# Kernel tuning notes

Measured on AMD Instinct MI355X. Metric: run time of the kernel, lower is better.

The kernel has to match this reference:

```python
import jax, jax.numpy as jnp
import numpy as np

L, B, T, F, C, H, DFF = 2, 4, 2048, 1024, 200, 8, 128


def setup_inputs() -> dict:
    key = jax.random.key(0)
    ks = jax.random.split(key, 12)
    s = 0.02
    return {
        "x": jax.random.normal(ks[0], (B, T, F), jnp.float32),
        "prototypes": jax.random.normal(ks[1], (C, 1, F), jnp.float32),
        # conv_query / conv_key (1x1 convs == linear), per RAB layer
        "wq": jax.random.normal(ks[2], (L, F, F), jnp.float32) * s,
        "bq": jnp.zeros((L, F), jnp.float32),
        "wk": jax.random.normal(ks[3], (L, F, F), jnp.float32) * s,
        "bk": jnp.zeros((L, F), jnp.float32),
        # nn.MultiheadAttention packed in-proj and out-proj
        "in_w": jax.random.normal(ks[4], (L, 3 * F, F), jnp.float32) * s,
        "in_b": jnp.zeros((L, 3 * F), jnp.float32),
        "out_w": jax.random.normal(ks[5], (L, F, F), jnp.float32) * s,
        "out_b": jnp.zeros((L, F), jnp.float32),
        # FFN
        "l1_w": jax.random.normal(ks[6], (L, DFF, F), jnp.float32) * s,
        "l1_b": jnp.zeros((L, DFF), jnp.float32),
        "l2_w": jax.random.normal(ks[7], (L, F, DFF), jnp.float32) * s,
        "l2_b": jnp.zeros((L, F), jnp.float32),
        # LayerNorms
        "ln1_g": jnp.ones((L, F), jnp.float32),
        "ln1_b": jnp.zeros((L, F), jnp.float32),
        "ln2_g": jnp.ones((L, F), jnp.float32),
        "ln2_b": jnp.zeros((L, F), jnp.float32),
        # feature_embedding: Conv1d(F, F, k=3, pad=1) + ReLU
        "emb_w": jax.random.normal(ks[8], (F, F, 3), jnp.float32) * s,
        "emb_b": jnp.zeros((F,), jnp.float32),
    }


def _ln(x, g, b, eps=1e-5):
    mu = jnp.mean(x, axis=-1, keepdims=True)
    var = jnp.mean((x - mu) ** 2, axis=-1, keepdims=True)
    return (x - mu) * jax.lax.rsqrt(var + eps) * g + b


def _mha(q, k, v, w, b, ow, ob):
    # q,k,v: (B,S,F). Packed in-proj like nn.MultiheadAttention (eval: no dropout).
    f = q.shape[-1]
    dh = f // H
    Q = q @ w[:f].T + b[:f]
    K = k @ w[f:2 * f].T + b[f:2 * f]
    V = v @ w[2 * f:].T + b[2 * f:]
    sp = lambda t: t.reshape(t.shape[0], t.shape[1], H, dh)
    scale = np.float32(1.0 / np.sqrt(dh))
    att = jnp.einsum('bqhd,bkhd->bhqk', sp(Q), sp(K)) * scale
    att = jax.nn.softmax(att, axis=-1)
    o = jnp.einsum('bhqk,bkhd->bqhd', att, sp(V)).reshape(q.shape)
    return o @ ow.T + ob


def reference(x, prototypes, wq, bq, wk, bk, in_w, in_b, out_w, out_b,
              l1_w, l1_b, l2_w, l2_b, ln1_g, ln1_b, ln2_g, ln2_b, emb_w, emb_b):
    Bn, Tn, Fn = x.shape
    # torch: prototypes.view(1, F, -1)  (a reshape, NOT a transpose)
    proto = jnp.broadcast_to(prototypes.reshape(1, Fn, -1), (Bn, Fn, prototypes.shape[0]))
    # concat along time: (B,F,S) with S = T + C, then work in (B,S,F)
    src = jnp.swapaxes(jnp.concatenate([jnp.swapaxes(x, 1, 2), proto], axis=2), 1, 2)
    for l in range(L):
        q = src @ wq[l].T + bq[l]          # conv1x1 == pointwise linear
        k = src @ wk[l].T + bk[l]
        a = _mha(q, k, src, in_w[l], in_b[l], out_w[l], out_b[l])
        src = _ln(src + a, ln1_g[l], ln1_b[l])
        ff = jax.nn.relu(src @ l1_w[l].T + l1_b[l]) @ l2_w[l].T + l2_b[l]
        src = _ln(src + ff, ln2_g[l], ln2_b[l])
    feat = jnp.swapaxes(src[:, :Tn], 1, 2)  # (B,F,T): drop prototype tokens
    y = jax.lax.conv_general_dilated(feat, emb_w, (1,), ((1, 1),),
                                     dimension_numbers=('NCH', 'OIH', 'NCH'))
    return jax.nn.relu(y + emb_b[None, :, None])
```

## Files before the change

### kernel.cpp

```cpp
#include <hip/hip_runtime.h>
#include <hip/hip_bf16.h>


constexpr int BN = 4, TN = 2048, FD = 1024, CP = 200, SN = TN + CP;
constexpr int HN = 8, DH = 128, DF = 128, MR = BN * SN;
constexpr int SF = 3 * FD;
constexpr int NT = (SN + 63) / 64;
constexpr float C2 = 0.12751744f;

typedef __attribute__((ext_vector_type(8))) short short8;
typedef __attribute__((ext_vector_type(4))) float f32x4;

__device__ __forceinline__ ushort f2b(float f) {
  union { float f; uint u; } v{f};
  return (ushort)((v.u + 0x7fffu + ((v.u >> 16) & 1u)) >> 16);
}
__device__ __forceinline__ float b2f(ushort u) {
  union { uint u; float f; } v{(uint)u << 16};
  return v.f;
}
__device__ __forceinline__ uint cvt_pk_bf16(float a, float b) {
  uint r;
  asm("v_cvt_pk_bf16_f32 %0, %1, %2" : "=v"(r) : "v"(a), "v"(b));
  return r;
}
__device__ __forceinline__ float exp2_fast(float x) {
  float r;
  asm("v_exp_f32 %0, %1" : "=v"(r) : "v"(x));
  return r;
}
__device__ __forceinline__ void gld16(const void* g, void* l) {
  __builtin_amdgcn_global_load_lds(
      (const __attribute__((address_space(1))) void*)g,
      (__attribute__((address_space(3))) void*)l, 16, 0, 0);
}

__global__ __launch_bounds__(256) void k_build(const float* __restrict__ x,
                                               const float* __restrict__ proto,
                                               ushort* __restrict__ srcb) {
  const int row = blockIdx.x;
  const int b = row / SN, s = row % SN;
  const int f = threadIdx.x * 4;
  const size_t o = (size_t)row * FD + f;
  float4 v;
  if (s < TN) {
    v = *(const float4*)(x + ((size_t)b * TN + s) * FD + f);
  } else {
    const int c = s - TN;
    v.x = proto[(size_t)(f + 0) * CP + c];
    v.y = proto[(size_t)(f + 1) * CP + c];
    v.z = proto[(size_t)(f + 2) * CP + c];
    v.w = proto[(size_t)(f + 3) * CP + c];
  }
  ushort4 u{f2b(v.x), f2b(v.y), f2b(v.z), f2b(v.w)};
  *(ushort4*)(srcb + o) = u;
}

__global__ __launch_bounds__(256) void k_cvt(const float* __restrict__ in,
                                             ushort* __restrict__ out, int n) {
  const int n4 = n >> 2;
  for (int i = blockIdx.x * 256 + threadIdx.x; i < n4; i += gridDim.x * 256) {
    const float4 v = *(const float4*)(in + (size_t)i * 4);
    ushort4 u{f2b(v.x), f2b(v.y), f2b(v.z), f2b(v.w)};
    *(ushort4*)(out + (size_t)i * 4) = u;
  }
}

__global__ __launch_bounds__(256) void k_cvt_inw(const float* __restrict__ in,
                                                 ushort* __restrict__ wInQK,
                                                 ushort* __restrict__ wQKV) {
  constexpr size_t FF = (size_t)FD * FD;
  const int n4 = (int)(6 * FF / 4);
  for (int i = blockIdx.x * 256 + threadIdx.x; i < n4; i += gridDim.x * 256) {
    const size_t idx = (size_t)i * 4;
    const float4 v = *(const float4*)(in + idx);
    ushort4 u{f2b(v.x), f2b(v.y), f2b(v.z), f2b(v.w)};
    const int l = (int)(idx / (3 * FF));
    const size_t r = idx % (3 * FF);
    ushort* dst = (r >= 2 * FF) ? (wQKV + l * 3 * FF + r)
                                : (wInQK + l * 2 * FF + r);
    *(ushort4*)dst = u;
  }
}

__global__ __launch_bounds__(256) void k_cvtT(const float* __restrict__ wq,
                                              const float* __restrict__ wk,
                                              ushort* __restrict__ wT) {
  const int z = blockIdx.z;
  const int qk = z >> 1, l = z & 1;
  const float* W = (qk ? wk : wq) + (size_t)l * FD * FD;
  ushort* WT = wT + (size_t)z * FD * FD;
  __shared__ float t[32][33];
  const int tx = threadIdx.x & 31, ty = threadIdx.x >> 5;
  const int x0 = blockIdx.x * 32, y0 = blockIdx.y * 32;
#pragma unroll
  for (int dy = 0; dy < 4; ++dy)
    t[ty + dy * 8][tx] = W[(size_t)(y0 + ty + dy * 8) * FD + x0 + tx];
  __syncthreads();
#pragma unroll
  for (int dy = 0; dy < 4; ++dy)
    WT[(size_t)(x0 + ty + dy * 8) * FD + y0 + tx] = f2b(t[tx][ty + dy * 8]);
}

__global__ __launch_bounds__(256) void k_vT(const ushort* __restrict__ V,
                                            ushort* __restrict__ Vt) {
  __shared__ ushort t[32][34];
  const int tx = threadIdx.x & 31, ty = threadIdx.x >> 5;
  const int s0 = blockIdx.x * 32, d0 = blockIdx.y * 32, bh = blockIdx.z;
  const int b = bh >> 3, h = bh & 7;
#pragma unroll
  for (int dy = 0; dy < 4; ++dy) {
    const int s = min(s0 + ty + dy * 8, SN - 1);
    t[ty + dy * 8][tx] = V[((size_t)b * SN + s) * SF + h * DH + d0 + tx];
  }
  __syncthreads();
#pragma unroll
  for (int dy = 0; dy < 4; ++dy) {
    const int s = s0 + tx;
    if (s < SN)
      Vt[((size_t)bh * DH + d0 + ty + dy * 8) * SN + s] = t[tx][ty + dy * 8];
  }
}

__global__ __launch_bounds__(256) void k_convw(const float* __restrict__ W,
                                               ushort* __restrict__ out) {
  const int n = FD * FD * 3;
  for (int idx = blockIdx.x * 256 + threadIdx.x; idx < n;
       idx += gridDim.x * 256) {
    const int o = idx / (FD * 3);
    const int rem = idx % (FD * 3);
    const int tau = rem >> 10, i = rem & 1023;
    out[idx] = f2b(W[(size_t)o * (FD * 3) + i * 3 + tau]);
  }
}

__global__ __launch_bounds__(256) void k_pad(const ushort* __restrict__ sb,
                                             ushort* __restrict__ pad) {
  const int r = blockIdx.x, b = blockIdx.y;
  const int f = threadIdx.x * 4;
  ushort4 v{0, 0, 0, 0};
  if (r >= 1 && r <= TN)
    v = *(const ushort4*)(sb + ((size_t)b * SN + (r - 1)) * FD + f);
  *(ushort4*)(pad + ((size_t)b * (TN + 2) + r) * FD + f) = v;
}

__global__ __launch_bounds__(256) void k_beff(const float* __restrict__ in_w,
                                              const float* __restrict__ bvec,
                                              const float* __restrict__ in_b,
                                              float* __restrict__ out, int qk) {
  const int n = blockIdx.x, l = blockIdx.y, tid = threadIdx.x;
  const float* Win = in_w + (size_t)(l * 3 + qk) * FD * FD;
  const float* bv = bvec + (size_t)l * FD;
  float s = 0.f;
  for (int j = tid; j < FD; j += 256) s += Win[(size_t)n * FD + j] * bv[j];
  __shared__ float red[4];
#pragma unroll
  for (int o = 32; o; o >>= 1) s += __shfl_xor(s, o);
  if ((tid & 63) == 0) red[tid >> 6] = s;
  __syncthreads();
  if (tid == 0)
    out[l * 3 * FD + qk * FD + n] =
        red[0] + red[1] + red[2] + red[3] + in_b[l * 3 * FD + qk * FD + n];
}

__global__ __launch_bounds__(256) void k_copyv(const float* __restrict__ in_b,
                                               float* __restrict__ bqkv) {
  const int l = blockIdx.y;
  const int i = blockIdx.x * 256 + threadIdx.x;
  bqkv[l * 3 * FD + 2 * FD + i] = in_b[l * 3 * FD + 2 * FD + i];
}

template <bool RELU, bool BF16OUT, bool PREP4 = false>
__global__ __launch_bounds__(256) void k_mm(const ushort* __restrict__ A,
                                            const ushort* __restrict__ W,
                                            const float* __restrict__ bias,
                                            void* __restrict__ Cv,
                                            int M, int N, int K) {
  constexpr size_t FF = (size_t)FD * FD;
  if (PREP4) {
    const int z = blockIdx.z;
    A += (size_t)z * FF;
    W += (size_t)(((z & 1) * 2) + (z >> 1)) * FF;
    Cv = (void*)((ushort*)Cv + (size_t)((z >> 1) * 3 + (z & 1)) * FF);
  }
  __shared__ __align__(16) ushort As[128 * 32];
  __shared__ __align__(16) ushort Ws[128 * 32];
  const int tid = threadIdx.x;
  const int lane = tid & 63, wv = tid >> 6;
  const int l15 = lane & 15, g = lane >> 4;
  const int wr = wv >> 1, wc = wv & 1;
  int bx = blockIdx.x, by = blockIdx.y;
  const int nwg = gridDim.x * gridDim.y;
  if ((nwg & 7) == 0) {
    int bid = by * gridDim.x + bx;
    bid = (bid & 7) * (nwg >> 3) + (bid >> 3);
    bx = bid % gridDim.x;
    by = bid / gridDim.x;
  }
  const int m0 = by * 128, n0 = bx * 128;
  f32x4 acc[4][4];
#pragma unroll
  for (int i = 0; i < 4; ++i)
#pragma unroll
    for (int j = 0; j < 4; ++j) acc[i][j] = (f32x4){0.f, 0.f, 0.f, 0.f};

  for (int k0 = 0; k0 < K; k0 += 32) {
#pragma unroll
    for (int j = 0; j < 2; ++j) {
      const int u = j * 256 + wv * 64 + lane;
      const int r = u >> 2, c = (u & 3) * 8;
      const int gm = min(m0 + r, M - 1);
      gld16(A + (size_t)gm * K + k0 + c, As + (size_t)u * 8);
    }
#pragma unroll
    for (int j = 0; j < 2; ++j) {
      const int u = j * 256 + wv * 64 + lane;
      const int r = u >> 2, c = (u & 3) * 8;
      gld16(W + (size_t)(n0 + r) * K + k0 + c, Ws + (size_t)u * 8);
    }
    __syncthreads();
    short8 af[4], bfr[4];
#pragma unroll
    for (int i = 0; i < 4; ++i)
      af[i] = *(const short8*)(As + (wr * 64 + i * 16 + l15) * 32 + g * 8);
#pragma unroll
    for (int j = 0; j < 4; ++j)
      bfr[j] = *(const short8*)(Ws + (wc * 64 + j * 16 + l15) * 32 + g * 8);
    __builtin_amdgcn_s_setprio(1);
#pragma unroll
    for (int i = 0; i < 4; ++i)
#pragma unroll
      for (int j = 0; j < 4; ++j)
        acc[i][j] = __builtin_amdgcn_mfma_f32_16x16x32_bf16(af[i], bfr[j],
                                                            acc[i][j], 0, 0, 0);
    __builtin_amdgcn_s_setprio(0);
    __syncthreads();
  }
#pragma unroll
  for (int i = 0; i < 4; ++i) {
#pragma unroll
    for (int r = 0; r < 4; ++r) {
      const int row = m0 + wr * 64 + i * 16 + g * 4 + r;
      if (row >= M) continue;
#pragma unroll
      for (int j = 0; j < 4; ++j) {
        const int col = n0 + wc * 64 + j * 16 + l15;
        float v = acc[i][j][r];
        if (bias) v += bias[col];
        if (RELU) v = fmaxf(v, 0.f);
        if (BF16OUT)
          ((ushort*)Cv)[(size_t)row * N + col] = f2b(v);
        else
          ((float*)Cv)[(size_t)row * N + col] = v;
      }
    }
  }
}

template <bool CONV, bool BF16OUT>
__global__ __launch_bounds__(512, 1) void k_mmB(const ushort* __restrict__ A,
                                                const ushort* __restrict__ W,
                                                const float* __restrict__ bias,
                                                void* __restrict__ Cv,
                                                int M, int N, int K) {
  __shared__ __align__(16) ushort As[2][128 * 64];
  __shared__ __align__(16) ushort Bs[2][256 * 64];
  const int tid = threadIdx.x;
  const int lane = tid & 63, wv = tid >> 6;
  const int l15 = lane & 15, g = lane >> 4;
  const int wr = wv >> 2, wc = wv & 3;
  int bx = blockIdx.x, by = blockIdx.y;
  const int nwg = gridDim.x * gridDim.y;
  if ((nwg & 7) == 0) {
    int bid = by * gridDim.x + bx;
    bid = (bid & 7) * (nwg >> 3) + (bid >> 3);
    bx = bid % gridDim.x;
    by = bid / gridDim.x;
  }
  const int m0 = by * 128, n0 = bx * 256;
  const int NKt = K >> 6;

  f32x4 acc[4][4];
#pragma unroll
  for (int i = 0; i < 4; ++i)
#pragma unroll
    for (int j = 0; j < 4; ++j) acc[i][j] = (f32x4){0.f, 0.f, 0.f, 0.f};

  auto stage = [&](int kt, int d) {
    const int kb = kt * 64;
#pragma unroll
    for (int j = 0; j < 2; ++j) {
      const int u = j * 512 + tid;
      const int row = u >> 3, s = u & 7;
      const int c = s ^ (row & 7);
      const ushort* ga;
      if (CONV) {
        const int rm = m0 + row;
        const int bb = rm >> 11, tt = rm & 2047;
        ga = A + (size_t)(bb * (TN + 2) + tt + (kb >> 10)) * FD + (kb & 1023) +
             c * 8;
      } else {
        ga = A + (size_t)min(m0 + row, M - 1) * K + kb + c * 8;
      }
      gld16(ga, As[d] + row * 64 + s * 8);
    }
#pragma unroll
    for (int j = 0; j < 4; ++j) {
      const int u = j * 512 + tid;
      const int row = u >> 3, s = u & 7;
      const int c = s ^ (row & 7);
      gld16(W + (size_t)(n0 + row) * K + kb + c * 8, Bs[d] + row * 64 + s * 8);
    }
  };

  stage(0, 0);
  for (int kt = 0; kt < NKt; ++kt) {
    const int cur = kt & 1;
    if (kt + 1 < NKt) {
      stage(kt + 1, cur ^ 1);
      asm volatile("s_waitcnt vmcnt(6)" ::: "memory");
    } else {
      asm volatile("s_waitcnt vmcnt(0)" ::: "memory");
    }
    __builtin_amdgcn_s_barrier();
    __builtin_amdgcn_sched_barrier(0);
#pragma unroll
    for (int ks = 0; ks < 2; ++ks) {
      short8 aq[4], bq[4];
#pragma unroll
      for (int mf = 0; mf < 4; ++mf) {
        const int row = wr * 64 + mf * 16 + l15;
        aq[mf] = *(const short8*)(As[cur] + row * 64 +
                                  (((ks * 4 + g) ^ (row & 7)) << 3));
      }
#pragma unroll
      for (int nf = 0; nf < 4; ++nf) {
        const int row = wc * 64 + nf * 16 + l15;
        bq[nf] = *(const short8*)(Bs[cur] + row * 64 +
                                  (((ks * 4 + g) ^ (row & 7)) << 3));
      }
      __builtin_amdgcn_s_setprio(1);
#pragma unroll
      for (int mf = 0; mf < 4; ++mf)
#pragma unroll
        for (int nf = 0; nf < 4; ++nf)
          acc[mf][nf] = __builtin_amdgcn_mfma_f32_16x16x32_bf16(
              aq[mf], bq[nf], acc[mf][nf], 0, 0, 0);
      __builtin_amdgcn_s_setprio(0);
    }
    asm volatile("s_waitcnt lgkmcnt(0)" ::: "memory");
    __builtin_amdgcn_s_barrier();
  }

#pragma unroll
  for (int mf = 0; mf < 4; ++mf) {
#pragma unroll
    for (int r = 0; r < 4; ++r) {
      const int row = m0 + wr * 64 + mf * 16 + g * 4 + r;
      if (!CONV && row >= M) continue;
#pragma unroll
      for (int nf = 0; nf < 4; ++nf) {
        const int col = n0 + wc * 64 + nf * 16 + l15;
        float v = acc[mf][nf][r];
        if (bias) v += bias[col];
        if (CONV) {
          v = fmaxf(v, 0.f);
          const int bb = row >> 11, tt = row & 2047;
          ((float*)Cv)[((size_t)(bb * FD + col)) * TN + tt] = v;
        } else if (BF16OUT) {
          ((ushort*)Cv)[(size_t)row * N + col] = f2b(v);
        } else {
          ((float*)Cv)[(size_t)row * N + col] = v;
        }
      }
    }
  }
}

__global__ __launch_bounds__(512) void k_fattn(const ushort* __restrict__ Qg,
                                               const ushort* __restrict__ Kg,
                                               const ushort* __restrict__ Vt,
                                               ushort* __restrict__ Og) {
  __shared__ __align__(16) ushort Ks[64 * 128];
  __shared__ __align__(16) ushort Vs[128 * 64];
  __shared__ __align__(16) ushort Ps[8][16 * 64];
  const int tid = threadIdx.x, lane = tid & 63, wv = tid >> 6;
  const int l15 = lane & 15, g = lane >> 4;
  const int b = blockIdx.z, h = blockIdx.y, q0 = blockIdx.x * 128;
  const size_t rowBase = (size_t)b * SN;
  const int hoff = h * DH;
  const size_t vbase = (size_t)(b * HN + h) * DH * SN;

  short8 qf[4];
  const int qrow = min(q0 + wv * 16 + l15, SN - 1);
#pragma unroll
  for (int c = 0; c < 4; ++c)
    qf[c] = *(const short8*)(Qg + (rowBase + qrow) * SF + hoff + c * 32 + g * 8);

  short8 onesf;
#pragma unroll
  for (int i = 0; i < 8; ++i) onesf[i] = (short)0x3F80;

  f32x4 o[8];
#pragma unroll
  for (int dt = 0; dt < 8; ++dt) o[dt] = (f32x4){0.f, 0.f, 0.f, 0.f};
  f32x4 lacc = (f32x4){0.f, 0.f, 0.f, 0.f};
  const char* KsB = (const char*)Ks;
  const char* VsB = (const char*)Vs;
  char* PsB = (char*)&Ps[wv][0];

  for (int t = 0; t < NT; ++t) {
    const int kv0 = t * 64;
    const bool tl = (t == NT - 1);
    if (tl) {
#pragma unroll
      for (int j = 0; j < 2; ++j) {
        const int su = j * 512 + tid;
        const int row = su >> 4, s = su & 15;
        const int c16 = s ^ (row & 7);
        const int krow = min(kv0 + row, SN - 1);
        gld16(Kg + (rowBase + krow) * SF + hoff + c16 * 8, Ks + (size_t)su * 8);
      }
#pragma unroll
      for (int j = 0; j < 2; ++j) {
        const int su = j * 512 + tid;
        const int row = su >> 3, s = su & 7;
        const int cc = s ^ (row & 7);
        const int kvc = min(kv0 + cc * 8, SN - 8);
        gld16(Vt + vbase + (size_t)row * SN + kvc, Vs + (size_t)su * 8);
      }
    } else {
#pragma unroll
      for (int j = 0; j < 2; ++j) {
        const int su = j * 512 + tid;
        const int row = su >> 4, s = su & 15;
        const int c16 = s ^ (row & 7);
        gld16(Kg + (rowBase + kv0 + row) * SF + hoff + c16 * 8,
              Ks + (size_t)su * 8);
      }
#pragma unroll
      for (int j = 0; j < 2; ++j) {
        const int su = j * 512 + tid;
        const int row = su >> 3, s = su & 7;
        const int cc = s ^ (row & 7);
        gld16(Vt + vbase + (size_t)row * SN + kv0 + cc * 8,
              Vs + (size_t)su * 8);
      }
    }
    __syncthreads();

    f32x4 st[4];
    __builtin_amdgcn_s_setprio(1);
#pragma unroll
    for (int kt = 0; kt < 4; ++kt) {
      f32x4 s4 = (f32x4){0.f, 0.f, 0.f, 0.f};
      const int row = kt * 16 + l15;
#pragma unroll
      for (int c = 0; c < 4; ++c) {
        const short8 kf = *(const short8*)(
            KsB + row * 256 + (((c * 4 + g) ^ (row & 7)) << 4));
        s4 = __builtin_amdgcn_mfma_f32_16x16x32_bf16(kf, qf[c], s4, 0, 0, 0);
      }
      st[kt] = s4;
    }
    __builtin_amdgcn_s_setprio(0);

    float pfl[16];
    if (tl) {
#pragma unroll
      for (int kt = 0; kt < 4; ++kt)
#pragma unroll
        for (int r = 0; r < 4; ++r) {
          const int kvg = kv0 + kt * 16 + g * 4 + r;
          pfl[kt * 4 + r] = (kvg < SN) ? exp2_fast(C2 * st[kt][r]) : 0.f;
        }
    } else {
#pragma unroll
      for (int i = 0; i < 16; ++i)
        pfl[i] = exp2_fast(C2 * st[i >> 2][i & 3]);
    }

#pragma unroll
    for (int kt = 0; kt < 4; ++kt) {
      const uint lo = cvt_pk_bf16(pfl[kt * 4 + 0], pfl[kt * 4 + 1]);
      const uint hi = cvt_pk_bf16(pfl[kt * 4 + 2], pfl[kt * 4 + 3]);
      const int slot = (kt * 2 + (g >> 1)) ^ (l15 & 7);
      *(uint2*)(PsB + l15 * 128 + slot * 16 + (g & 1) * 8) = make_uint2(lo, hi);
    }

    __builtin_amdgcn_s_setprio(1);
#pragma unroll
    for (int c2 = 0; c2 < 2; ++c2) {
      const int pslot = (c2 * 4 + g) ^ (l15 & 7);
      const short8 pf = *(const short8*)(PsB + l15 * 128 + pslot * 16);
      lacc = __builtin_amdgcn_mfma_f32_16x16x32_bf16(pf, onesf, lacc, 0, 0, 0);
#pragma unroll
      for (int dt = 0; dt < 8; ++dt) {
        const int row = dt * 16 + l15;
        const short8 vf = *(const short8*)(
            VsB + row * 128 + (((c2 * 4 + g) ^ (row & 7)) << 4));
        o[dt] = __builtin_amdgcn_mfma_f32_16x16x32_bf16(pf, vf, o[dt], 0, 0, 0);
      }
    }
    __builtin_amdgcn_s_setprio(0);
    __syncthreads();
  }

  float ir[4];
#pragma unroll
  for (int r = 0; r < 4; ++r) ir[r] = 1.f / lacc[r];
#pragma unroll
  for (int r = 0; r < 4; ++r) {
    const int orow = q0 + wv * 16 + g * 4 + r;
    if (orow >= SN) continue;
#pragma unroll
    for (int dt = 0; dt < 8; ++dt)
      Og[(rowBase + orow) * FD + hoff + dt * 16 + l15] = f2b(o[dt][r] * ir[r]);
  }
}

__global__ __launch_bounds__(256) void k_add_ln(ushort* __restrict__ sb,
                                                const ushort* __restrict__ d,
                                                const float* __restrict__ g,
                                                const float* __restrict__ be) {
  __shared__ float red[4];
  const int row = blockIdx.x;
  const int tid = threadIdx.x;
  const int c = tid * 4;
  const size_t off = (size_t)row * FD + c;
  const ushort4 sv = *(const ushort4*)(sb + off);
  const ushort4 dv = *(const ushort4*)(d + off);
  float v[4] = {b2f(sv.x) + b2f(dv.x), b2f(sv.y) + b2f(dv.y),
                b2f(sv.z) + b2f(dv.z), b2f(sv.w) + b2f(dv.w)};
  float sum = v[0] + v[1] + v[2] + v[3];
#pragma unroll
  for (int o = 32; o; o >>= 1) sum += __shfl_xor(sum, o);
  if ((tid & 63) == 0) red[tid >> 6] = sum;
  __syncthreads();
  sum = red[0] + red[1] + red[2] + red[3];
  const float mu = sum * (1.f / FD);
  float vs = 0.f;
#pragma unroll
  for (int i = 0; i < 4; ++i) {
    const float t = v[i] - mu;
    vs += t * t;
  }
  __syncthreads();
#pragma unroll
  for (int o = 32; o; o >>= 1) vs += __shfl_xor(vs, o);
  if ((tid & 63) == 0) red[tid >> 6] = vs;
  __syncthreads();
  vs = red[0] + red[1] + red[2] + red[3];
  const float rstd = rsqrtf(vs * (1.f / FD) + 1e-5f);
  const float4 gv = *(const float4*)(g + c);
  const float4 bv = *(const float4*)(be + c);
  ushort4 u{f2b((v[0] - mu) * rstd * gv.x + bv.x),
            f2b((v[1] - mu) * rstd * gv.y + bv.y),
            f2b((v[2] - mu) * rstd * gv.z + bv.z),
            f2b((v[3] - mu) * rstd * gv.w + bv.w)};
  *(ushort4*)(sb + off) = u;
}

extern "C" void kernel_launch(void* const* d_in, const int* in_sizes, int n_in,
                              void* d_out, int out_size, void* d_ws,
                              size_t ws_size, hipStream_t stream) {
  const float* x      = (const float*)d_in[0];
  const float* proto  = (const float*)d_in[1];
  const float* wq     = (const float*)d_in[2];
  const float* bq     = (const float*)d_in[3];
  const float* wk     = (const float*)d_in[4];
  const float* bk     = (const float*)d_in[5];
  const float* in_w   = (const float*)d_in[6];
  const float* in_b   = (const float*)d_in[7];
  const float* out_w  = (const float*)d_in[8];
  const float* out_b  = (const float*)d_in[9];
  const float* l1_w   = (const float*)d_in[10];
  const float* l1_b   = (const float*)d_in[11];
  const float* l2_w   = (const float*)d_in[12];
  const float* l2_b   = (const float*)d_in[13];
  const float* ln1_g  = (const float*)d_in[14];
  const float* ln1_b  = (const float*)d_in[15];
  const float* ln2_g  = (const float*)d_in[16];
  const float* ln2_b  = (const float*)d_in[17];
  const float* emb_w  = (const float*)d_in[18];
  const float* emb_b  = (const float*)d_in[19];

  char* p = (char*)d_ws;
  auto take = [&](size_t bytes) {
    char* r = p;
    p += (bytes + 255) & ~(size_t)255;
    return r;
  };
  const size_t MF = (size_t)MR * FD;
  const size_t FF = (size_t)FD * FD;
  ushort* srcb  = (ushort*)take(MF * 2);
  ushort* bQKV  = (ushort*)take((size_t)MR * SF * 2);
  ushort* bVt   = (ushort*)take((size_t)BN * HN * DH * SN * 2);
  ushort* bO    = (ushort*)take(MF * 2);
  ushort* bFF   = (ushort*)take((size_t)MR * DF * 2);
  ushort* wQKV  = (ushort*)take((size_t)2 * 3 * FF * 2);
  ushort* wOut  = (ushort*)take((size_t)2 * FF * 2);
  ushort* wL1   = (ushort*)take((size_t)2 * DF * FD * 2);
  ushort* wL2   = (ushort*)take((size_t)2 * FD * DF * 2);
  float*  bqkv  = (float*)take((size_t)2 * SF * 4);
  ushort* wT     = bQKV;
  ushort* wInQK  = bQKV + 4 * FF;
  ushort* bOut   = bQKV;
  ushort* srcPad = bQKV;
  ushort* convW  = bQKV + (size_t)10 * 1024 * 1024;

  k_build<<<MR, 256, 0, stream>>>(x, proto, srcb);
  k_cvt_inw<<<2048, 256, 0, stream>>>(in_w, wInQK, wQKV);
  k_cvt<<<1024, 256, 0, stream>>>(out_w, wOut, 2 * FF);
  k_cvt<<<256, 256, 0, stream>>>(l1_w, wL1, 2 * DF * FD);
  k_cvt<<<256, 256, 0, stream>>>(l2_w, wL2, 2 * FD * DF);
  k_cvtT<<<dim3(32, 32, 4), 256, 0, stream>>>(wq, wk, wT);
  k_mm<false, true, true><<<dim3(8, 8, 4), 256, 0, stream>>>(
      wInQK, wT, nullptr, wQKV, FD, FD, FD);
  k_beff<<<dim3(FD, 2), 256, 0, stream>>>(in_w, bq, in_b, bqkv, 0);
  k_beff<<<dim3(FD, 2), 256, 0, stream>>>(in_w, bk, in_b, bqkv, 1);
  k_copyv<<<dim3(4, 2), 256, 0, stream>>>(in_b, bqkv);

  const int MB = (MR + 127) / 128;

  for (int l = 0; l < 2; ++l) {
    k_mmB<false, true><<<dim3(SF / 256, MB), 512, 0, stream>>>(
        srcb, wQKV + (size_t)l * 3 * FF, bqkv + (size_t)l * SF, bQKV, MR, SF,
        FD);
    k_vT<<<dim3((SN + 31) / 32, DH / 32, BN * HN), 256, 0, stream>>>(
        bQKV + 2 * FD, bVt);
    k_fattn<<<dim3((SN + 127) / 128, HN, BN), 512, 0, stream>>>(
        bQKV, bQKV + FD, bVt, bO);
    k_mmB<false, true><<<dim3(FD / 256, MB), 512, 0, stream>>>(
        bO, wOut + (size_t)l * FF, out_b + (size_t)l * FD, bOut, MR, FD, FD);
    k_add_ln<<<MR, 256, 0, stream>>>(srcb, bOut, ln1_g + (size_t)l * FD,
                                     ln1_b + (size_t)l * FD);
    k_mm<true, true><<<dim3(DF / 128, MB), 256, 0, stream>>>(
        srcb, wL1 + (size_t)l * DF * FD, l1_b + (size_t)l * DF, bFF, MR, DF,
        FD);
    k_mm<false, true><<<dim3(FD / 128, MB), 256, 0, stream>>>(
        bFF, wL2 + (size_t)l * FD * DF, l2_b + (size_t)l * FD, bOut, MR, FD,
        DF);
    k_add_ln<<<MR, 256, 0, stream>>>(srcb, bOut, ln2_g + (size_t)l * FD,
                                     ln2_b + (size_t)l * FD);
  }

  k_convw<<<1024, 256, 0, stream>>>(emb_w, convW);
  k_pad<<<dim3(TN + 2, BN), 256, 0, stream>>>(srcb, srcPad);
  k_mmB<true, false><<<dim3(FD / 256, (BN * TN) / 128), 512, 0, stream>>>(
      srcPad, convW, emb_b, (float*)d_out, BN * TN, FD, 3 * FD);
}
```

Before: 0.9997 ms.

## Replace double-buffered 128x256 GEMM with simple 128x128 kernel and retile attention

Removes the 512-thread double-buffered k_mmB GEMM and routes the QKV, out-projection and conv GEMMs through the simpler single-buffered 256-thread 128x128 k_mm, which gains a CONV addressing mode. Flash attention moves from 128-query/512-thread blocks to 64-query/256-thread blocks, with an XCD-aware block remap so each (batch, head) group lands on one XCD. The bias kernels are merged into one launch. The changes trade software pipelining and larger tiles for more blocks and better cache locality, at the risk of exposing more global-load latency in the large GEMMs.

```diff
diff --git a/kernel.cpp b/kernel.cpp
--- a/kernel.cpp
+++ b/kernel.cpp
@@ -145,12 +145,19 @@
 }
 
 __global__ __launch_bounds__(256) void k_beff(const float* __restrict__ in_w,
-                                              const float* __restrict__ bvec,
+                                              const float* __restrict__ bq,
+                                              const float* __restrict__ bk,
                                               const float* __restrict__ in_b,
-                                              float* __restrict__ out, int qk) {
-  const int n = blockIdx.x, l = blockIdx.y, tid = threadIdx.x;
+                                              float* __restrict__ out) {
+  const int n = blockIdx.x, l = blockIdx.y, qk = blockIdx.z;
+  const int tid = threadIdx.x;
+  if (qk == 2) {
+    if (tid == 0)
+      out[l * 3 * FD + 2 * FD + n] = in_b[l * 3 * FD + 2 * FD + n];
+    return;
+  }
   const float* Win = in_w + (size_t)(l * 3 + qk) * FD * FD;
-  const float* bv = bvec + (size_t)l * FD;
+  const float* bv = (qk ? bk : bq) + (size_t)l * FD;
   float s = 0.f;
   for (int j = tid; j < FD; j += 256) s += Win[(size_t)n * FD + j] * bv[j];
   __shared__ float red[4];
@@ -163,14 +170,7 @@
         red[0] + red[1] + red[2] + red[3] + in_b[l * 3 * FD + qk * FD + n];
 }
 
-__global__ __launch_bounds__(256) void k_copyv(const float* __restrict__ in_b,
-                                               float* __restrict__ bqkv) {
-  const int l = blockIdx.y;
-  const int i = blockIdx.x * 256 + threadIdx.x;
-  bqkv[l * 3 * FD + 2 * FD + i] = in_b[l * 3 * FD + 2 * FD + i];
-}
-
-template <bool RELU, bool BF16OUT, bool PREP4 = false>
+template <bool RELU, bool BF16OUT, bool PREP4 = false, bool CONV = false>
 __global__ __launch_bounds__(256) void k_mm(const ushort* __restrict__ A,
                                             const ushort* __restrict__ W,
                                             const float* __restrict__ bias,
@@ -209,8 +209,16 @@
     for (int j = 0; j < 2; ++j) {
       const int u = j * 256 + wv * 64 + lane;
       const int r = u >> 2, c = (u & 3) * 8;
-      const int gm = min(m0 + r, M - 1);
-      gld16(A + (size_t)gm * K + k0 + c, As + (size_t)u * 8);
+      const ushort* ga;
+      if (CONV) {
+        const int rm = m0 + r;
+        const int bb = rm >> 11, tt = rm & 2047;
+        ga = A + (size_t)(bb * (TN + 2) + tt + (k0 >> 10)) * FD + (k0 & 1023) +
+             c;
+      } else {
+        ga = A + (size_t)min(m0 + r, M - 1) * K + k0 + c;
+      }
+      gld16(ga, As + (size_t)u * 8);
     }
 #pragma unroll
     for (int j = 0; j < 2; ++j) {
@@ -241,130 +249,14 @@
 #pragma unroll
     for (int r = 0; r < 4; ++r) {
       const int row = m0 + wr * 64 + i * 16 + g * 4 + r;
-      if (row >= M) continue;
+      if (!CONV && row >= M) continue;
 #pragma unroll
       for (int j = 0; j < 4; ++j) {
         const int col = n0 + wc * 64 + j * 16 + l15;
         float v = acc[i][j][r];
         if (bias) v += bias[col];
-        if (RELU) v = fmaxf(v, 0.f);
-        if (BF16OUT)
-          ((ushort*)Cv)[(size_t)row * N + col] = f2b(v);
-        else
-          ((float*)Cv)[(size_t)row * N + col] = v;
-      }
-    }
-  }
-}
-
-template <bool CONV, bool BF16OUT>
-__global__ __launch_bounds__(512, 1) void k_mmB(const ushort* __restrict__ A,
-                                                const ushort* __restrict__ W,
-                                                const float* __restrict__ bias,
-                                                void* __restrict__ Cv,
-                                                int M, int N, int K) {
-  __shared__ __align__(16) ushort As[2][128 * 64];
-  __shared__ __align__(16) ushort Bs[2][256 * 64];
-  const int tid = threadIdx.x;
-  const int lane = tid & 63, wv = tid >> 6;
-  const int l15 = lane & 15, g = lane >> 4;
-  const int wr = wv >> 2, wc = wv & 3;
-  int bx = blockIdx.x, by = blockIdx.y;
-  const int nwg = gridDim.x * gridDim.y;
-  if ((nwg & 7) == 0) {
-    int bid = by * gridDim.x + bx;
-    bid = (bid & 7) * (nwg >> 3) + (bid >> 3);
-    bx = bid % gridDim.x;
-    by = bid / gridDim.x;
-  }
-  const int m0 = by * 128, n0 = bx * 256;
-  const int NKt = K >> 6;
-
-  f32x4 acc[4][4];
-#pragma unroll
-  for (int i = 0; i < 4; ++i)
-#pragma unroll
-    for (int j = 0; j < 4; ++j) acc[i][j] = (f32x4){0.f, 0.f, 0.f, 0.f};
-
-  auto stage = [&](int kt, int d) {
-    const int kb = kt * 64;
-#pragma unroll
-    for (int j = 0; j < 2; ++j) {
-      const int u = j * 512 + tid;
-      const int row = u >> 3, s = u & 7;
-      const int c = s ^ (row & 7);
-      const ushort* ga;
-      if (CONV) {
-        const int rm = m0 + row;
-        const int bb = rm >> 11, tt = rm & 2047;
-        ga = A + (size_t)(bb * (TN + 2) + tt + (kb >> 10)) * FD + (kb & 1023) +
-             c * 8;
-      } else {
-        ga = A + (size_t)min(m0 + row, M - 1) * K + kb + c * 8;
-      }
-      gld16(ga, As[d] + row * 64 + s * 8);
-    }
-#pragma unroll
-    for (int j = 0; j < 4; ++j) {
-      const int u = j * 512 + tid;
-      const int row = u >> 3, s = u & 7;
-      const int c = s ^ (row & 7);
-      gld16(W + (size_t)(n0 + row) * K + kb + c * 8, Bs[d] + row * 64 + s * 8);
-    }
-  };
-
-  stage(0, 0);
-  for (int kt = 0; kt < NKt; ++kt) {
-    const int cur = kt & 1;
-    if (kt + 1 < NKt) {
-      stage(kt + 1, cur ^ 1);
-      asm volatile("s_waitcnt vmcnt(6)" ::: "memory");
-    } else {
-      asm volatile("s_waitcnt vmcnt(0)" ::: "memory");
-    }
-    __builtin_amdgcn_s_barrier();
-    __builtin_amdgcn_sched_barrier(0);
-#pragma unroll
-    for (int ks = 0; ks < 2; ++ks) {
-      short8 aq[4], bq[4];
-#pragma unroll
-      for (int mf = 0; mf < 4; ++mf) {
-        const int row = wr * 64 + mf * 16 + l15;
-        aq[mf] = *(const short8*)(As[cur] + row * 64 +
-                                  (((ks * 4 + g) ^ (row & 7)) << 3));
-      }
-#pragma unroll
-      for (int nf = 0; nf < 4; ++nf) {
-        const int row = wc * 64 + nf * 16 + l15;
-        bq[nf] = *(const short8*)(Bs[cur] + row * 64 +
-                                  (((ks * 4 + g) ^ (row & 7)) << 3));
-      }
-      __builtin_amdgcn_s_setprio(1);
-#pragma unroll
-      for (int mf = 0; mf < 4; ++mf)
-#pragma unroll
-        for (int nf = 0; nf < 4; ++nf)
-          acc[mf][nf] = __builtin_amdgcn_mfma_f32_16x16x32_bf16(
-              aq[mf], bq[nf], acc[mf][nf], 0, 0, 0);
-      __builtin_amdgcn_s_setprio(0);
-    }
-    asm volatile("s_waitcnt lgkmcnt(0)" ::: "memory");
-    __builtin_amdgcn_s_barrier();
-  }
-
-#pragma unroll
-  for (int mf = 0; mf < 4; ++mf) {
-#pragma unroll
-    for (int r = 0; r < 4; ++r) {
-      const int row = m0 + wr * 64 + mf * 16 + g * 4 + r;
-      if (!CONV && row >= M) continue;
-#pragma unroll
-      for (int nf = 0; nf < 4; ++nf) {
-        const int col = n0 + wc * 64 + nf * 16 + l15;
-        float v = acc[mf][nf][r];
-        if (bias) v += bias[col];
+        if (RELU || CONV) v = fmaxf(v, 0.f);
         if (CONV) {
-          v = fmaxf(v, 0.f);
           const int bb = row >> 11, tt = row & 2047;
           ((float*)Cv)[((size_t)(bb * FD + col)) * TN + tt] = v;
         } else if (BF16OUT) {
@@ -377,19 +269,23 @@
   }
 }
 
-__global__ __launch_bounds__(512) void k_fattn(const ushort* __restrict__ Qg,
+__global__ __launch_bounds__(256) void k_fattn(const ushort* __restrict__ Qg,
                                                const ushort* __restrict__ Kg,
                                                const ushort* __restrict__ Vt,
                                                ushort* __restrict__ Og) {
   __shared__ __align__(16) ushort Ks[64 * 128];
   __shared__ __align__(16) ushort Vs[128 * 64];
-  __shared__ __align__(16) ushort Ps[8][16 * 64];
+  __shared__ __align__(16) ushort Ps[4][16 * 64];
   const int tid = threadIdx.x, lane = tid & 63, wv = tid >> 6;
   const int l15 = lane & 15, g = lane >> 4;
-  const int b = blockIdx.z, h = blockIdx.y, q0 = blockIdx.x * 128;
+  const int flat = blockIdx.x + NT * (blockIdx.y + HN * blockIdx.z);
+  const int xcd = flat & 7, slot = flat >> 3;
+  const int grp = xcd + 8 * (slot / NT);
+  const int qt = slot % NT;
+  const int b = grp >> 3, h = grp & 7, q0 = qt * 64;
   const size_t rowBase = (size_t)b * SN;
   const int hoff = h * DH;
-  const size_t vbase = (size_t)(b * HN + h) * DH * SN;
+  const size_t vbase = (size_t)grp * DH * SN;
 
   short8 qf[4];
   const int qrow = min(q0 + wv * 16 + l15, SN - 1);
@@ -414,16 +310,16 @@
     const bool tl = (t == NT - 1);
     if (tl) {
 #pragma unroll
-      for (int j = 0; j < 2; ++j) {
-        const int su = j * 512 + tid;
+      for (int j = 0; j < 4; ++j) {
+        const int su = j * 256 + tid;
         const int row = su >> 4, s = su & 15;
         const int c16 = s ^ (row & 7);
         const int krow = min(kv0 + row, SN - 1);
         gld16(Kg + (rowBase + krow) * SF + hoff + c16 * 8, Ks + (size_t)su * 8);
       }
 #pragma unroll
-      for (int j = 0; j < 2; ++j) {
-        const int su = j * 512 + tid;
+      for (int j = 0; j < 4; ++j) {
+        const int su = j * 256 + tid;
         const int row = su >> 3, s = su & 7;
         const int cc = s ^ (row & 7);
         const int kvc = min(kv0 + cc * 8, SN - 8);
@@ -431,16 +327,16 @@
       }
     } else {
 #pragma unroll
-      for (int j = 0; j < 2; ++j) {
-        const int su = j * 512 + tid;
+      for (int j = 0; j < 4; ++j) {
+        const int su = j * 256 + tid;
         const int row = su >> 4, s = su & 15;
         const int c16 = s ^ (row & 7);
         gld16(Kg + (rowBase + kv0 + row) * SF + hoff + c16 * 8,
               Ks + (size_t)su * 8);
       }
 #pragma unroll
-      for (int j = 0; j < 2; ++j) {
-        const int su = j * 512 + tid;
+      for (int j = 0; j < 4; ++j) {
+        const int su = j * 256 + tid;
         const int row = su >> 3, s = su & 7;
         const int cc = s ^ (row & 7);
         gld16(Vt + vbase + (size_t)row * SN + kv0 + cc * 8,
@@ -617,21 +513,18 @@
   k_cvtT<<<dim3(32, 32, 4), 256, 0, stream>>>(wq, wk, wT);
   k_mm<false, true, true><<<dim3(8, 8, 4), 256, 0, stream>>>(
       wInQK, wT, nullptr, wQKV, FD, FD, FD);
-  k_beff<<<dim3(FD, 2), 256, 0, stream>>>(in_w, bq, in_b, bqkv, 0);
-  k_beff<<<dim3(FD, 2), 256, 0, stream>>>(in_w, bk, in_b, bqkv, 1);
-  k_copyv<<<dim3(4, 2), 256, 0, stream>>>(in_b, bqkv);
+  k_beff<<<dim3(FD, 2, 3), 256, 0, stream>>>(in_w, bq, bk, in_b, bqkv);
 
   const int MB = (MR + 127) / 128;
 
   for (int l = 0; l < 2; ++l) {
-    k_mmB<false, true><<<dim3(SF / 256, MB), 512, 0, stream>>>(
+    k_mm<false, true><<<dim3(SF / 128, MB), 256, 0, stream>>>(
         srcb, wQKV + (size_t)l * 3 * FF, bqkv + (size_t)l * SF, bQKV, MR, SF,
         FD);
     k_vT<<<dim3((SN + 31) / 32, DH / 32, BN * HN), 256, 0, stream>>>(
         bQKV + 2 * FD, bVt);
-    k_fattn<<<dim3((SN + 127) / 128, HN, BN), 512, 0, stream>>>(
-        bQKV, bQKV + FD, bVt, bO);
-    k_mmB<false, true><<<dim3(FD / 256, MB), 512, 0, stream>>>(
+    k_fattn<<<dim3(NT, HN, BN), 256, 0, stream>>>(bQKV, bQKV + FD, bVt, bO);
+    k_mm<false, true><<<dim3(FD / 128, MB), 256, 0, stream>>>(
         bO, wOut + (size_t)l * FF, out_b + (size_t)l * FD, bOut, MR, FD, FD);
     k_add_ln<<<MR, 256, 0, stream>>>(srcb, bOut, ln1_g + (size_t)l * FD,
                                      ln1_b + (size_t)l * FD);
@@ -647,6 +540,8 @@
 
   k_convw<<<1024, 256, 0, stream>>>(emb_w, convW);
   k_pad<<<dim3(TN + 2, BN), 256, 0, stream>>>(srcb, srcPad);
-  k_mmB<true, false><<<dim3(FD / 256, (BN * TN) / 128), 512, 0, stream>>>(
-      srcPad, convW, emb_b, (float*)d_out, BN * TN, FD, 3 * FD);
-}
+  k_mm<true, false, false, true><<<dim3(FD / 128, (BN * TN) / 128), 256, 0,
+                                   stream>>>(srcPad, convW, emb_b,
+                                             (float*)d_out, BN * TN, FD,
+                                             3 * FD);
+}
```

New measurement: 915.1 us. 8.5% less time.
